# Optimization experiments

Measured on AMD Instinct MI355X. Metric: run time of the kernel, lower is better.

Reference implementation:

```python
import jax, jax.numpy as jnp
import numpy as np

H = 12  # num_heads
LN_EPS = 1e-5


def setup_inputs() -> dict:
    key = jax.random.key(0)
    ks = jax.random.split(key, 9)
    B, N, C = 16, 785, 768
    hd = C // H
    s = lambda k, shp, fan: jax.random.normal(k, shp, jnp.float32) * (1.0 / np.sqrt(fan))
    return {
        "x": jax.random.normal(ks[0], (B, N, C), jnp.float32),
        "qkv_w": s(ks[1], (C, 3 * C), C),          # Linear(dim, 3*dim), no bias
        "proj_w": s(ks[2], (C, C), C),
        "proj_b": jnp.zeros((C,), jnp.float32),
        "htp_w": s(ks[3], (hd, C), hd),            # ht_proj: Linear(hd, dim)
        "htp_b": jnp.zeros((C,), jnp.float32),
        "ln_g": jnp.ones((hd,), jnp.float32),      # ht_norm LayerNorm(hd)
        "ln_b": jnp.zeros((hd,), jnp.float32),
        "pos": jax.random.normal(ks[4], (1, H, C), jnp.float32) * 0.02,
    }


def reference(x, qkv_w, proj_w, proj_b, htp_w, htp_b, ln_g, ln_b, pos):
    B, N, C = x.shape
    hd = C // H
    scale = hd ** -0.5

    # head-token construction: per-head mean pool over tokens -> (B, H, hd)
    xh = x.reshape(B, N, H, hd).mean(axis=1)
    ht = (xh @ htp_w + htp_b).reshape(B, H, H, hd)        # ht_proj then split per head
    mu = ht.mean(axis=-1, keepdims=True)
    var = ht.var(axis=-1, keepdims=True)
    ht = (ht - mu) * jax.lax.rsqrt(var + LN_EPS) * ln_g + ln_b
    ht = jax.nn.gelu(ht, approximate=False).reshape(B, H, C) + pos  # + head pos embed

    xa = jnp.concatenate([x, ht], axis=1)                 # (B, T, C), T = N + H
    T = N + H

    qkv = (xa @ qkv_w).reshape(B, T, 3, H, hd)
    q, k, v = (jnp.moveaxis(qkv, 2, 0)[i].transpose(0, 2, 1, 3) for i in range(3))  # (B,H,T,hd)
    attn = jax.nn.softmax(jnp.einsum("bhqd,bhkd->bhqk", q, k) * scale, axis=-1)
    out = jnp.einsum("bhqk,bhkd->bhqd", attn, v).transpose(0, 2, 1, 3).reshape(B, T, C)
    out = out @ proj_w + proj_b

    cls = out[:, :1] + out[:, N:].mean(axis=1, keepdims=True)  # cls += mean of head tokens
    return jnp.concatenate([cls, out[:, 1:N]], axis=1)         # (B, N, C)
```

## Files before the change

### kernel.cpp

```cpp
#include <hip/hip_runtime.h>
#include <hip/hip_bf16.h>
#include <math.h>

#define Bsz 16
#define Ntok 785
#define Cdim 768
#define Hn 12
#define HD 64
#define Ttok 797
#define Kdim 768
#define K3C 2304
#define LN_EPS 1e-5f
#define Mrows (Bsz * Ttok)
#define NQS 3
#define NPARTS 5

typedef _Float16 f16;
typedef __attribute__((ext_vector_type(8))) _Float16 half8;
typedef __attribute__((ext_vector_type(4))) _Float16 half4v;
typedef __attribute__((ext_vector_type(8))) unsigned short ushort8;
typedef __attribute__((ext_vector_type(4))) float f32x4;

__device__ inline float wave_sum(float v) {
    #pragma unroll
    for (int off = 32; off; off >>= 1) v += __shfl_xor(v, off, 64);
    return v;
}

#define SW(row) (((((row) & 7) ^ (((row) >> 3) & 7))) << 3)

__global__ void prep_x(const float* __restrict__ x, f16* __restrict__ xa,
                       float* __restrict__ partial) {
    int b = blockIdx.x, ch = blockIdx.y, t = threadIdx.x;
    int n0 = ch * 50, n1 = min(Ntok, n0 + 50);
    float s0 = 0.f, s1 = 0.f, s2 = 0.f;
    for (int n = n0; n < n1; ++n) {
        const float* row = x + ((size_t)b * Ntok + n) * Cdim;
        f16* orow = xa + ((size_t)b * Ttok + n) * Cdim;
        float v0 = row[t], v1 = row[t + 256], v2 = row[t + 512];
        s0 += v0; s1 += v1; s2 += v2;
        orow[t] = (f16)v0; orow[t + 256] = (f16)v1; orow[t + 512] = (f16)v2;
    }
    float* p = partial + ((size_t)b * 16 + ch) * Cdim;
    p[t] = s0; p[t + 256] = s1; p[t + 512] = s2;
}

__global__ void headtok_kernel(const float* __restrict__ partial, const float* __restrict__ htp_w,
                               const float* __restrict__ htp_b, const float* __restrict__ ln_g,
                               const float* __restrict__ ln_b, const float* __restrict__ pos,
                               f16* __restrict__ xa) {
    int blk = blockIdx.x;
    int b  = blk / (Hn * Hn);
    int rem = blk % (Hn * Hn);
    int h  = rem / Hn;
    int h2 = rem % Hn;
    int lane = threadIdx.x;
    int c = h2 * HD + lane;

    float sx = 0.f;
    #pragma unroll
    for (int ch = 0; ch < 16; ++ch)
        sx += partial[((size_t)b * 16 + ch) * Cdim + h * HD + lane];
    float xv = sx * (1.0f / (float)Ntok);

    float acc = htp_b[c];
    #pragma unroll 8
    for (int d = 0; d < HD; ++d) acc += __shfl(xv, d, 64) * htp_w[(size_t)d * Cdim + c];

    float mu = wave_sum(acc) * (1.0f / 64.0f);
    float diff = acc - mu;
    float var = wave_sum(diff * diff) * (1.0f / 64.0f);
    float y = diff * rsqrtf(var + LN_EPS) * ln_g[lane] + ln_b[lane];
    float g = 0.5f * y * (1.0f + erff(y * 0.70710678118654752f));
    float v = g + pos[(size_t)h * Cdim + c];
    xa[((size_t)b * Ttok + Ntok + h) * Cdim + c] = (f16)v;
}

__global__ void convert_both(const float* __restrict__ Wq, f16* __restrict__ WTq,
                             const float* __restrict__ Wp, f16* __restrict__ WTp) {
    __shared__ float tile[32][33];
    int bx = blockIdx.x;
    const float* W; f16* WT; int N, nt;
    if (bx < K3C / 32) { W = Wq; WT = WTq; N = K3C; nt = bx * 32; }
    else               { W = Wp; WT = WTp; N = Cdim; nt = (bx - K3C / 32) * 32; }
    int kt = blockIdx.y * 32;
    int tx = threadIdx.x & 31, ty = threadIdx.x >> 5;
    #pragma unroll
    for (int r = 0; r < 32; r += 8)
        tile[ty + r][tx] = W[(size_t)(kt + ty + r) * N + nt + tx];
    __syncthreads();
    #pragma unroll
    for (int r = 0; r < 32; r += 8) {
        int n = nt + ty + r, k = kt + tx;
        WT[(size_t)n * Kdim + k] = (f16)tile[tx][ty + r];
    }
}

__global__ __launch_bounds__(256, 3)
void mfma_gemm(const f16* __restrict__ A, const f16* __restrict__ W,
               const float* __restrict__ bias, int M, int Nn, int mode, int nNb,
               float* __restrict__ outF, float* __restrict__ sbuf,
               f16* __restrict__ outH) {
    __shared__ __align__(16) f16 smem[3][2][4096];
    const int idx = blockIdx.x;
    const int xcd = idx & 7;
    const int sidx = idx >> 3;
    const int mloc = sidx % 13;
    const int nb = sidx / 13;
    const int cnt = (xcd < 4) ? 13 : 12;
    if (mloc >= cnt) return;
    const int mb = (xcd < 4 ? xcd * 13 : 52 + (xcd - 4) * 12) + mloc;
    const int mBase = mb * 128, nBase = nb * 128;

    const int tid = threadIdx.x;
    const int w = tid >> 6, lane = tid & 63;
    const int lr = lane & 15, lg = lane >> 4;
    const int wr = w >> 1, wc = w & 1;

    const f16* src = (w < 2) ? A : W;
    const int arr = w >> 1;
    const int rowOff = (w & 1) * 64;
    const int rowBase = (w < 2) ? mBase : nBase;
    const int rowMax  = (w < 2) ? (M - 1) : (Nn - 1);
    const int cg = (lane & 3) ^ ((lane >> 2) & 3);
    const int sl8 = (lg ^ (lr & 3)) * 8;

    f32x4 acc[4][4];
    #pragma unroll
    for (int mi = 0; mi < 4; ++mi)
        #pragma unroll
        for (int ni = 0; ni < 4; ++ni) {
            acc[mi][ni][0] = 0.f; acc[mi][ni][1] = 0.f;
            acc[mi][ni][2] = 0.f; acc[mi][ni][3] = 0.f;
        }

    auto stage = [&](int buf, int k0) {
        #pragma unroll
        for (int i = 0; i < 4; ++i) {
            int r16 = rowOff + i * 16;
            int grow = min(rowBase + r16 + (lane >> 2), rowMax);
            const f16* g = src + (size_t)grow * Kdim + k0 + cg * 8;
            f16* l = &smem[buf][arr][r16 * 32];
            __builtin_amdgcn_global_load_lds(
                (const __attribute__((address_space(1))) void*)g,
                (__attribute__((address_space(3))) void*)l, 16, 0, 0);
        }
    };

    const int NT = Kdim / 32;
    stage(0, 0);
    stage(1, 32);
    asm volatile("s_waitcnt vmcnt(4)" ::: "memory");
    __builtin_amdgcn_sched_barrier(0);
    __builtin_amdgcn_s_barrier();
    __builtin_amdgcn_sched_barrier(0);

    int cur = 0;
    for (int t = 0; t < NT; ++t) {
        if (t + 2 < NT) {
            int nbuf = cur + 2; if (nbuf >= 3) nbuf -= 3;
            stage(nbuf, (t + 2) * 32);
        }
        const f16* AS = &smem[cur][0][0];
        const f16* WS = &smem[cur][1][0];
        half8 a[4], b[4];
        #pragma unroll
        for (int mi = 0; mi < 4; ++mi)
            a[mi] = *reinterpret_cast<const half8*>(&AS[(wr * 64 + mi * 16 + lr) * 32 + sl8]);
        #pragma unroll
        for (int ni = 0; ni < 4; ++ni)
            b[ni] = *reinterpret_cast<const half8*>(&WS[(wc * 64 + ni * 16 + lr) * 32 + sl8]);
        #pragma unroll
        for (int mi = 0; mi < 4; ++mi)
            #pragma unroll
            for (int ni = 0; ni < 4; ++ni)
                acc[mi][ni] = __builtin_amdgcn_mfma_f32_16x16x32_f16(a[mi], b[ni], acc[mi][ni], 0, 0, 0);

        if (t + 1 < NT) {
            if (t + 2 < NT)
                asm volatile("s_waitcnt vmcnt(4) lgkmcnt(0)" ::: "memory");
            else
                asm volatile("s_waitcnt vmcnt(0) lgkmcnt(0)" ::: "memory");
            __builtin_amdgcn_sched_barrier(0);
            __builtin_amdgcn_s_barrier();
            __builtin_amdgcn_sched_barrier(0);
        }
        cur = cur + 1; if (cur >= 3) cur -= 3;
    }

    if (mode == 0) {
        #pragma unroll
        for (int ni = 0; ni < 4; ++ni) {
            int gn = nBase + wc * 64 + ni * 16 + lr;
            float bv = bias ? bias[gn] : 0.f;
            #pragma unroll
            for (int mi = 0; mi < 4; ++mi)
                #pragma unroll
                for (int r = 0; r < 4; ++r) {
                    int gm = mBase + wr * 64 + mi * 16 + lg * 4 + r;
                    if (gm < M) {
                        int bb = gm / Ttok, tt = gm - bb * Ttok;
                        float v = acc[mi][ni][r] + bv;
                        if (tt >= 1 && tt < Ntok)
                            outF[((size_t)bb * Ntok + tt) * Nn + gn] = v;
                        else
                            sbuf[((size_t)bb * 13 + (tt == 0 ? 0 : tt - Ntok + 1)) * Nn + gn] = v;
                    }
                }
        }
    } else {
        __syncthreads();
        f16* Ew = &smem[0][0][0] + (size_t)w * 4096;
        #pragma unroll
        for (int mi = 0; mi < 4; ++mi)
            #pragma unroll
            for (int ni = 0; ni < 4; ++ni)
                #pragma unroll
                for (int r = 0; r < 4; ++r) {
                    int er = mi * 16 + lg * 4 + r;
                    int ec = ni * 16 + lr;
                    int chunk = ec >> 3;
                    Ew[er * 64 + ((chunk ^ (er & 7)) << 3) + (ec & 7)] = (f16)acc[mi][ni][r];
                }
        __syncthreads();
        int scol = nBase + wc * 64;
        int s = scol / Cdim;
        int hc = scol - s * Cdim;
        int h = hc >> 6;
        #pragma unroll
        for (int c8 = 0; c8 < 8; ++c8) {
            int er = (lane >> 3) + c8 * 8;
            int chunk = lane & 7;
            half8 v = *reinterpret_cast<const half8*>(&Ew[er * 64 + ((chunk ^ (er & 7)) << 3)]);
            int gm = mBase + wr * 64 + er;
            if (gm < M) {
                int bb = gm / Ttok, tt = gm - bb * Ttok;
                f16* dst = outH + (((size_t)(s * Bsz + bb) * Hn + h) * Ttok + tt) * HD + chunk * 8;
                *reinterpret_cast<half8*>(dst) = v;
            }
        }
    }
}

__global__ __launch_bounds__(256, 2)
void flash_attn_kernel(const f16* __restrict__ Qb, const f16* __restrict__ Kb,
                       const f16* __restrict__ Vb, f16* __restrict__ ao) {
    __shared__ __align__(16) unsigned short KS[64 * 64];
    __shared__ __align__(16) unsigned short VS[64 * 64];

    int bh   = blockIdx.x / NPARTS;
    int part = blockIdx.x % NPARTS;
    int q0 = part * (NQS * 64);
    int smax = min(NQS, (Ttok - q0 + 63) / 64);
    int tid = threadIdx.x;
    int w = tid >> 6, lane = tid & 63;
    int lr = lane & 15, lg = lane >> 4;
    size_t base = (size_t)bh * Ttok * HD;

    half8 qf[NQS][2];
    #pragma unroll
    for (int s = 0; s < NQS; ++s) {
        int qrow = q0 + s * 64 + w * 16 + lr;
        int crow = min(qrow, Ttok - 1);
        #pragma unroll
        for (int kf = 0; kf < 2; ++kf)
            qf[s][kf] = *reinterpret_cast<const half8*>(Qb + base + (size_t)crow * HD + kf * 32 + lg * 8);
    }

    f32x4 O[NQS][4];
    float lsum[NQS];
    #pragma unroll
    for (int s = 0; s < NQS; ++s) {
        lsum[s] = 0.f;
        #pragma unroll
        for (int nt = 0; nt < 4; ++nt) { O[s][nt][0]=0.f; O[s][nt][1]=0.f; O[s][nt][2]=0.f; O[s][nt][3]=0.f; }
    }

    const unsigned short* Kg = (const unsigned short*)(Kb + base);
    const unsigned short* Vg = (const unsigned short*)(Vb + base);

    int pr = tid >> 3;
    int g  = tid & 7;

    for (int kt = 0; kt < 13; ++kt) {
        bool tail = (kt == 12);
        __syncthreads();
        {
            int k0 = 2 * pr, k1 = k0 + 1;
            int gk0 = kt * 64 + k0;
            ushort8 kv0, kv1, vv0, vv1;
            if (!tail) {
                kv0 = *reinterpret_cast<const ushort8*>(&Kg[(size_t)gk0 * HD + g * 8]);
                vv0 = *reinterpret_cast<const ushort8*>(&Vg[(size_t)gk0 * HD + g * 8]);
                kv1 = *reinterpret_cast<const ushort8*>(&Kg[(size_t)(gk0 + 1) * HD + g * 8]);
                vv1 = *reinterpret_cast<const ushort8*>(&Vg[(size_t)(gk0 + 1) * HD + g * 8]);
            } else {
                ushort8 z;
                #pragma unroll
                for (int jj = 0; jj < 8; ++jj) z[jj] = 0;
                kv0 = z; vv0 = z; kv1 = z; vv1 = z;
                if (gk0 < Ttok) {
                    kv0 = *reinterpret_cast<const ushort8*>(&Kg[(size_t)gk0 * HD + g * 8]);
                    vv0 = *reinterpret_cast<const ushort8*>(&Vg[(size_t)gk0 * HD + g * 8]);
                }
                if (gk0 + 1 < Ttok) {
                    kv1 = *reinterpret_cast<const ushort8*>(&Kg[(size_t)(gk0 + 1) * HD + g * 8]);
                    vv1 = *reinterpret_cast<const ushort8*>(&Vg[(size_t)(gk0 + 1) * HD + g * 8]);
                }
            }
            *reinterpret_cast<ushort8*>(&KS[(k0 * 64 + g * 8) ^ SW(k0)]) = kv0;
            *reinterpret_cast<ushort8*>(&KS[(k1 * 64 + g * 8) ^ SW(k1)]) = kv1;
            unsigned* VTd = reinterpret_cast<unsigned*>(VS);
            #pragma unroll
            for (int jj = 0; jj < 8; ++jj) {
                int dim = g * 8 + jj;
                unsigned w2 = (unsigned)vv0[jj] | ((unsigned)vv1[jj] << 16);
                VTd[dim * 32 + (pr ^ ((((dim & 7) ^ ((dim >> 3) & 7))) << 2))] = w2;
            }
        }
        __syncthreads();

        int kbase = kt * 64;
        #pragma unroll
        for (int s = 0; s < NQS; ++s) {
            if (s < smax) {
                half4v pa[4];
                float ls = 0.f;
                #pragma unroll
                for (int ntk = 0; ntk < 4; ++ntk) {
                    f32x4 sc; sc[0]=0.f; sc[1]=0.f; sc[2]=0.f; sc[3]=0.f;
                    #pragma unroll
                    for (int kf = 0; kf < 2; ++kf) {
                        int key = ntk * 16 + lr;
                        int d0 = kf * 32 + lg * 8;
                        half8 k8 = *reinterpret_cast<const half8*>(
                            reinterpret_cast<const f16*>(&KS[(key * 64 + d0) ^ SW(key)]));
                        sc = __builtin_amdgcn_mfma_f32_16x16x32_f16(k8, qf[s][kf], sc, 0, 0, 0);
                    }
                    float p[4];
                    if (!tail) {
                        #pragma unroll
                        for (int r = 0; r < 4; ++r) {
                            p[r] = __expf(sc[r] * 0.125f - 6.0f);
                            ls += p[r];
                        }
                    } else {
                        int kb2 = kbase + ntk * 16 + lg * 4;
                        #pragma unroll
                        for (int r = 0; r < 4; ++r) {
                            bool valid = (kb2 + r) < Ttok;
                            p[r] = valid ? __expf(sc[r] * 0.125f - 6.0f) : 0.f;
                            ls += p[r];
                        }
                    }
                    auto lo = __builtin_amdgcn_cvt_pkrtz(p[0], p[1]);
                    auto hi = __builtin_amdgcn_cvt_pkrtz(p[2], p[3]);
                    pa[ntk][0] = (f16)lo[0]; pa[ntk][1] = (f16)lo[1];
                    pa[ntk][2] = (f16)hi[0]; pa[ntk][3] = (f16)hi[1];
                }
                lsum[s] += ls;
                #pragma unroll
                for (int ntd = 0; ntd < 4; ++ntd) {
                    int dim = ntd * 16 + lr;
                    #pragma unroll
                    for (int ntk = 0; ntk < 4; ++ntk) {
                        half4v v4 = *reinterpret_cast<const half4v*>(
                            reinterpret_cast<const f16*>(&VS[(dim * 64 + ntk * 16 + lg * 4) ^ SW(dim)]));
                        O[s][ntd] = __builtin_amdgcn_mfma_f32_16x16x16f16(pa[ntk], v4, O[s][ntd], 0, 0, 0);
                    }
                }
            }
        }
    }

    __syncthreads();
    int b = bh / Hn, h = bh % Hn;
    f16* Ew = reinterpret_cast<f16*>(&KS[(size_t)w * 1024]);
    #pragma unroll
    for (int s = 0; s < NQS; ++s) {
        if (s < smax) {
            float l = lsum[s];
            l += __shfl_xor(l, 16, 64);
            l += __shfl_xor(l, 32, 64);
            float inv[4];
            #pragma unroll
            for (int r = 0; r < 4; ++r)
                inv[r] = 1.0f / __shfl(l, lg * 4 + r, 64);
            #pragma unroll
            for (int nt = 0; nt < 4; ++nt)
                #pragma unroll
                for (int r = 0; r < 4; ++r)
                    Ew[(lg * 4 + r) * 64 + nt * 16 + lr] = (f16)(O[s][nt][r] * inv[r]);
            int row = lane >> 2, seg = lane & 3;
            half8 v0 = *reinterpret_cast<const half8*>(&Ew[row * 64 + seg * 16]);
            half8 v1 = *reinterpret_cast<const half8*>(&Ew[row * 64 + seg * 16 + 8]);
            int qrow = q0 + s * 64 + w * 16 + row;
            if (qrow < Ttok) {
                f16* dst = ao + ((size_t)b * Ttok + qrow) * Cdim + h * HD + seg * 16;
                *reinterpret_cast<half8*>(dst) = v0;
                *reinterpret_cast<half8*>(dst + 8) = v1;
            }
        }
    }
}

__global__ void cls2_kernel(const float* __restrict__ sbuf, float* __restrict__ out) {
    int b = blockIdx.x, t = threadIdx.x;
    #pragma unroll
    for (int i = 0; i < 3; ++i) {
        int c = t + i * 256;
        float s = sbuf[((size_t)b * 13) * Cdim + c];
        float hs = 0.f;
        #pragma unroll
        for (int h = 0; h < Hn; ++h)
            hs += sbuf[((size_t)b * 13 + 1 + h) * Cdim + c];
        out[((size_t)b * Ntok) * Cdim + c] = s + hs * (1.0f / (float)Hn);
    }
}

extern "C" void kernel_launch(void* const* d_in, const int* in_sizes, int n_in,
                              void* d_out, int out_size, void* d_ws, size_t ws_size,
                              hipStream_t stream) {
    const float* x      = (const float*)d_in[0];
    const float* qkv_w  = (const float*)d_in[1];
    const float* proj_w = (const float*)d_in[2];
    const float* proj_b = (const float*)d_in[3];
    const float* htp_w  = (const float*)d_in[4];
    const float* htp_b  = (const float*)d_in[5];
    const float* ln_g   = (const float*)d_in[6];
    const float* ln_b   = (const float*)d_in[7];
    const float* pos    = (const float*)d_in[8];
    float* out = (float*)d_out;

    const size_t MC = (size_t)Mrows * Cdim;
    const size_t WQ = (size_t)K3C * Kdim;
    const size_t WP = (size_t)Cdim * Kdim;

    f16* qkv   = (f16*)d_ws;
    f16* xa    = qkv + 3 * MC;
    f16* wq    = xa + MC;
    f16* wp    = wq + WQ;
    float* partial = (float*)(wp + WP);
    float* sbuf    = partial + (size_t)Bsz * 16 * Cdim;

    prep_x<<<dim3(Bsz, 16), 256, 0, stream>>>(x, xa, partial);
    headtok_kernel<<<Bsz * Hn * Hn, 64, 0, stream>>>(partial, htp_w, htp_b, ln_g, ln_b, pos, xa);
    convert_both<<<dim3(96, Kdim / 32), 256, 0, stream>>>(qkv_w, wq, proj_w, wp);

    mfma_gemm<<<8 * 13 * 18, 256, 0, stream>>>(
        xa, wq, nullptr, Mrows, K3C, 1, 18, nullptr, nullptr, qkv);

    flash_attn_kernel<<<Bsz * Hn * NPARTS, 256, 0, stream>>>(
        qkv, qkv + MC, qkv + 2 * MC, xa);

    mfma_gemm<<<8 * 13 * 6, 256, 0, stream>>>(
        xa, wp, proj_b, Mrows, Cdim, 0, 6, out, sbuf, nullptr);

    cls2_kernel<<<Bsz, 256, 0, stream>>>(sbuf, out);
}
```

Measured before the change: 197.6 us.

## Double-buffer K/V LDS tiles in flash attention with register prefetch

The single LDS K/V buffer becomes two. The next tile's global loads are issued into registers while the current tile is computed, and the tile is written into the alternate buffer afterwards. This leaves one barrier per iteration instead of two and hides global load latency behind MFMA work. The query-block partition also changes so the last part handles two 64-row blocks, recomputing block 11 redundantly. The cost is double the LDS footprint, which may affect occupancy, plus extra live registers for the prefetched tile.

```diff
diff --git a/kernel.cpp b/kernel.cpp
--- a/kernel.cpp
+++ b/kernel.cpp
@@ -245,13 +245,14 @@
 __global__ __launch_bounds__(256, 2)
 void flash_attn_kernel(const f16* __restrict__ Qb, const f16* __restrict__ Kb,
                        const f16* __restrict__ Vb, f16* __restrict__ ao) {
-    __shared__ __align__(16) unsigned short KS[64 * 64];
-    __shared__ __align__(16) unsigned short VS[64 * 64];
+    __shared__ __align__(16) unsigned short KS[2][64 * 64];
+    __shared__ __align__(16) unsigned short VS[2][64 * 64];
 
     int bh   = blockIdx.x / NPARTS;
     int part = blockIdx.x % NPARTS;
-    int q0 = part * (NQS * 64);
-    int smax = min(NQS, (Ttok - q0 + 63) / 64);
+    int st   = 3 * part - (part == 4 ? 1 : 0);
+    int q0   = st * 64;
+    int smax = (part < 3) ? 3 : 2;
     int tid = threadIdx.x;
     int w = tid >> 6, lane = tid & 63;
     int lr = lane & 15, lg = lane >> 4;
@@ -281,44 +282,56 @@
 
     int pr = tid >> 3;
     int g  = tid & 7;
+    int k0 = 2 * pr, k1 = k0 + 1;
+
+    ushort8 kv0, kv1, vv0, vv1;
+    auto load_tile = [&](int kt) {
+        int gk0 = kt * 64 + k0;
+        if (kt < 12) {
+            kv0 = *reinterpret_cast<const ushort8*>(&Kg[(size_t)gk0 * HD + g * 8]);
+            vv0 = *reinterpret_cast<const ushort8*>(&Vg[(size_t)gk0 * HD + g * 8]);
+            kv1 = *reinterpret_cast<const ushort8*>(&Kg[(size_t)(gk0 + 1) * HD + g * 8]);
+            vv1 = *reinterpret_cast<const ushort8*>(&Vg[(size_t)(gk0 + 1) * HD + g * 8]);
+        } else {
+            ushort8 z;
+            #pragma unroll
+            for (int jj = 0; jj < 8; ++jj) z[jj] = 0;
+            kv0 = z; vv0 = z; kv1 = z; vv1 = z;
+            if (gk0 < Ttok) {
+                kv0 = *reinterpret_cast<const ushort8*>(&Kg[(size_t)gk0 * HD + g * 8]);
+                vv0 = *reinterpret_cast<const ushort8*>(&Vg[(size_t)gk0 * HD + g * 8]);
+            }
+            if (gk0 + 1 < Ttok) {
+                kv1 = *reinterpret_cast<const ushort8*>(&Kg[(size_t)(gk0 + 1) * HD + g * 8]);
+                vv1 = *reinterpret_cast<const ushort8*>(&Vg[(size_t)(gk0 + 1) * HD + g * 8]);
+            }
+        }
+    };
+    auto write_tile = [&](int buf) {
+        *reinterpret_cast<ushort8*>(&KS[buf][(k0 * 64 + g * 8) ^ SW(k0)]) = kv0;
+        *reinterpret_cast<ushort8*>(&KS[buf][(k1 * 64 + g * 8) ^ SW(k1)]) = kv1;
+        unsigned* VTd = reinterpret_cast<unsigned*>(&VS[buf][0]);
+        #pragma unroll
+        for (int jj = 0; jj < 8; ++jj) {
+            int dim = g * 8 + jj;
+            unsigned w2 = (unsigned)vv0[jj] | ((unsigned)vv1[jj] << 16);
+            VTd[dim * 32 + (pr ^ ((((dim & 7) ^ ((dim >> 3) & 7))) << 2))] = w2;
+        }
+    };
+
+    load_tile(0);
+    write_tile(0);
+    load_tile(1);
+    asm volatile("s_waitcnt lgkmcnt(0)" ::: "memory");
+    __builtin_amdgcn_sched_barrier(0);
+    __builtin_amdgcn_s_barrier();
+    __builtin_amdgcn_sched_barrier(0);
 
     for (int kt = 0; kt < 13; ++kt) {
         bool tail = (kt == 12);
-        __syncthreads();
-        {
-            int k0 = 2 * pr, k1 = k0 + 1;
-            int gk0 = kt * 64 + k0;
-            ushort8 kv0, kv1, vv0, vv1;
-            if (!tail) {
-                kv0 = *reinterpret_cast<const ushort8*>(&Kg[(size_t)gk0 * HD + g * 8]);
-                vv0 = *reinterpret_cast<const ushort8*>(&Vg[(size_t)gk0 * HD + g * 8]);
-                kv1 = *reinterpret_cast<const ushort8*>(&Kg[(size_t)(gk0 + 1) * HD + g * 8]);
-                vv1 = *reinterpret_cast<const ushort8*>(&Vg[(size_t)(gk0 + 1) * HD + g * 8]);
-            } else {
-                ushort8 z;
-                #pragma unroll
-                for (int jj = 0; jj < 8; ++jj) z[jj] = 0;
-                kv0 = z; vv0 = z; kv1 = z; vv1 = z;
-                if (gk0 < Ttok) {
-                    kv0 = *reinterpret_cast<const ushort8*>(&Kg[(size_t)gk0 * HD + g * 8]);
-                    vv0 = *reinterpret_cast<const ushort8*>(&Vg[(size_t)gk0 * HD + g * 8]);
-                }
-                if (gk0 + 1 < Ttok) {
-                    kv1 = *reinterpret_cast<const ushort8*>(&Kg[(size_t)(gk0 + 1) * HD + g * 8]);
-                    vv1 = *reinterpret_cast<const ushort8*>(&Vg[(size_t)(gk0 + 1) * HD + g * 8]);
-                }
-            }
-            *reinterpret_cast<ushort8*>(&KS[(k0 * 64 + g * 8) ^ SW(k0)]) = kv0;
-            *reinterpret_cast<ushort8*>(&KS[(k1 * 64 + g * 8) ^ SW(k1)]) = kv1;
-            unsigned* VTd = reinterpret_cast<unsigned*>(VS);
-            #pragma unroll
-            for (int jj = 0; jj < 8; ++jj) {
-                int dim = g * 8 + jj;
-                unsigned w2 = (unsigned)vv0[jj] | ((unsigned)vv1[jj] << 16);
-                VTd[dim * 32 + (pr ^ ((((dim & 7) ^ ((dim >> 3) & 7))) << 2))] = w2;
-            }
-        }
-        __syncthreads();
+        int cur = kt & 1;
+        const unsigned short* KSc = &KS[cur][0];
+        const unsigned short* VSc = &VS[cur][0];
 
         int kbase = kt * 64;
         #pragma unroll
@@ -334,7 +347,7 @@
                         int key = ntk * 16 + lr;
                         int d0 = kf * 32 + lg * 8;
                         half8 k8 = *reinterpret_cast<const half8*>(
-                            reinterpret_cast<const f16*>(&KS[(key * 64 + d0) ^ SW(key)]));
+                            reinterpret_cast<const f16*>(&KSc[(key * 64 + d0) ^ SW(key)]));
                         sc = __builtin_amdgcn_mfma_f32_16x16x32_f16(k8, qf[s][kf], sc, 0, 0, 0);
                     }
                     float p[4];
@@ -365,17 +378,26 @@
                     #pragma unroll
                     for (int ntk = 0; ntk < 4; ++ntk) {
                         half4v v4 = *reinterpret_cast<const half4v*>(
-                            reinterpret_cast<const f16*>(&VS[(dim * 64 + ntk * 16 + lg * 4) ^ SW(dim)]));
+                            reinterpret_cast<const f16*>(&VSc[(dim * 64 + ntk * 16 + lg * 4) ^ SW(dim)]));
                         O[s][ntd] = __builtin_amdgcn_mfma_f32_16x16x16f16(pa[ntk], v4, O[s][ntd], 0, 0, 0);
                     }
                 }
             }
         }
+
+        if (kt + 1 < 13) {
+            write_tile((kt + 1) & 1);
+            if (kt + 2 < 13) load_tile(kt + 2);
+            asm volatile("s_waitcnt lgkmcnt(0)" ::: "memory");
+            __builtin_amdgcn_sched_barrier(0);
+            __builtin_amdgcn_s_barrier();
+            __builtin_amdgcn_sched_barrier(0);
+        }
     }
 
     __syncthreads();
     int b = bh / Hn, h = bh % Hn;
-    f16* Ew = reinterpret_cast<f16*>(&KS[(size_t)w * 1024]);
+    f16* Ew = reinterpret_cast<f16*>(&KS[0][(size_t)w * 1024]);
     #pragma unroll
     for (int s = 0; s < NQS; ++s) {
         if (s < smax) {
```

New measurement: 191.0 us. 3.3% less time.
